# Performance work log

Measured on AMD Instinct MI355X. Metric: run time of the kernel, lower is better.

The kernel has to match this reference:

```python
import jax, jax.numpy as jnp
import numpy as np

# norse default LIFParameters (dt=1e-3): tau_mem_inv=100, tau_syn_inv=200, v_leak=0, v_reset=0
DT = 1e-3
TAU_MEM_INV = 100.0
TAU_SYN_INV = 200.0
V_TH_ENC = 1.0   # encoder built with default LIFParameters -> v_th=1.0
V_TH = 0.33      # LIF cells built with v_th=0.33
SEQ_LEN = 24
ALPHA = 100.0    # SuperSpike surrogate-gradient slope (norse 'super' method)

@jax.custom_vjp
def heaviside(x):
    # forward: hard threshold; backward: SuperSpike surrogate 1/(alpha*|x|+1)^2
    return (x > 0).astype(x.dtype)

def _hv_fwd(x):
    return heaviside(x), x

def _hv_bwd(x, g):
    return (g / (ALPHA * jnp.abs(x) + 1.0) ** 2,)

heaviside.defvjp(_hv_fwd, _hv_bwd)


def setup_inputs() -> dict:
    key = jax.random.key(0)
    ks = jax.random.split(key, 6)
    B, F, H, C = 4096, 1024, 256, 10
    def lin(k, fan_out, fan_in):  # torch Linear default init (no bias)
        bound = 1.0 / np.sqrt(fan_in)
        return jax.random.uniform(k, (fan_out, fan_in), jnp.float32, -bound, bound)
    return {
        "x": jax.random.normal(ks[0], (B, F), jnp.float32),
        "W1": lin(ks[1], H, F),
        "W2": lin(ks[2], H, H),
        "W3": lin(ks[3], H, H),
        "Wout": jax.random.normal(ks[4], (C, H), jnp.float32) * np.sqrt(2.0 / H),
        "feature_scalar": jnp.ones((1,), jnp.float32),
        "encoder_scalar": jnp.ones((1,), jnp.float32),
    }


def _lif_step(z_in, v, i):
    # norse lif_feed_forward_step: decay v/i from old state, spike, reset, then inject input into i
    v_dec = v + DT * TAU_MEM_INV * (-v + i)
    i_dec = i * (1.0 - DT * TAU_SYN_INV)
    z = heaviside(v_dec - V_TH)
    v_new = (1.0 - z) * v_dec  # v_reset = 0
    i_new = i_dec + z_in
    return z, v_new, i_new


def reference(x, W1, W2, W3, Wout, feature_scalar, encoder_scalar):
    B, F = x.shape
    H = W1.shape[0]
    C = Wout.shape[0]
    current = 2.0 * feature_scalar * x  # constant injected current, [B, F]
    z0 = lambda d: jnp.zeros((B, d), x.dtype)
    init = (z0(F), z0(H), z0(H), z0(H), z0(H), z0(H), z0(H), z0(C), z0(C))

    def step(state, _):
        v_enc, v1, i1, v2, i2, v3, i3, v_li, i_li = state
        # ConstantCurrentLIFEncoder (lif_current_encoder, v_th=1.0)
        v_enc = v_enc + DT * TAU_MEM_INV * (-v_enc + current)
        s = heaviside(v_enc - V_TH_ENC)
        v_enc = v_enc - s * v_enc  # reset to 0
        z = 5.0 * encoder_scalar * s
        # three Linear(no bias)+LIF stages (dropout in eval mode = identity)
        z, v1, i1 = _lif_step(1.2 * (z @ W1.T), v1, i1)
        z, v2, i2 = _lif_step(1.2 * (z @ W2.T), v2, i2)
        z, v3, i3 = _lif_step(1.2 * (z @ W3.T), v3, i3)
        # LILinearCell: leaky integrator readout
        v_li = v_li + DT * TAU_MEM_INV * (-v_li + i_li)
        i_li = i_li * (1.0 - DT * TAU_SYN_INV) + z @ Wout.T
        return (v_enc, v1, i1, v2, i2, v3, i3, v_li, i_li), None

    final, _ = jax.lax.scan(step, init, None, length=SEQ_LEN)
    return final[7]  # decode = voltages[-1], shape [B, n_classes]
```

## Files before the change

kernel.cpp:

```cpp
#include <hip/hip_runtime.h>

using u16 = unsigned short;
using u32 = unsigned int;
using u64 = unsigned long long;

typedef _Float16 half8 __attribute__((ext_vector_type(8)));
typedef float  f32x4 __attribute__((ext_vector_type(4)));
typedef u32    u32x4 __attribute__((ext_vector_type(4)));
typedef u32    u32x2 __attribute__((ext_vector_type(2)));

#define T_STEPS 24
#define NB 4096
#define NF 1024
#define NH 256
#define NCLS 10

static __device__ __forceinline__ void f16split(float w, u16& hi, u16& lo) {
  _Float16 h = (_Float16)w;
  float hf = (float)h;
  if (__builtin_fabsf(hf) < 6.103515625e-05f) { h = (_Float16)0.0f; hf = 0.0f; }
  float r = __fmul_rn(__fsub_rn(w, hf), 4096.0f);
  _Float16 l = (_Float16)r;
  hi = __builtin_bit_cast(u16, h);
  lo = __builtin_bit_cast(u16, l);
}

__global__ __launch_bounds__(256) void k_prep(const float* __restrict__ W1,
                                              const float* __restrict__ W2,
                                              const float* __restrict__ W3,
                                              u16* __restrict__ W1hl,
                                              u16* __restrict__ W2hl,
                                              u16* __restrict__ W3hl) {
  int blk = blockIdx.x, tid = threadIdx.x;
  const float* src; u16* dst; int K; int g;
  if (blk < 1024)      { src = W1; dst = W1hl; K = 1024; g = blk * 256 + tid; }
  else if (blk < 1280) { src = W2; dst = W2hl; K = 256;  g = (blk - 1024) * 256 + tid; }
  else                 { src = W3; dst = W3hl; K = 256;  g = (blk - 1280) * 256 + tid; }
  int n = g / K, k = g - n * K;
  u16 hi, lo;
  f16split(src[g], hi, lo);
  int p = k >> 6, j = k & 63;
  u16* d = dst + (size_t)n * 2 * K + p * 128 + j;
  d[0] = hi;
  d[64] = lo;
}

template <int NSC, int ASTRIDE>
__device__ __forceinline__ void mega_phase(u16* __restrict__ Bs,
                                           const u32* __restrict__ alds,
                                           const u16* __restrict__ wsrc,
                                           u32* __restrict__ zdst,
                                           float scale,
                                           int wid, int lane, int wm, int wn) {
  constexpr int KTOT = NSC * 32;
  constexpr int NG   = NSC / 4;

  const int q   = lane >> 4;
  const int bsh = q * 8;

  const u16* gs = wsrc + (size_t)(wid * 32 + (lane >> 2)) * KTOT + (lane & 3) * 8;
  const int sdst = wid * 1024;

  auto stage = [&](int s) {
    const int slot = s & 3;
    const u16* g = gs + s * 32;
    #pragma unroll
    for (int r = 0; r < 2; ++r)
      __builtin_amdgcn_global_load_lds(
          (const __attribute__((address_space(1))) u32*)(g + (size_t)r * 16 * KTOT),
          (__attribute__((address_space(3))) u32*)&Bs[slot * 8192 + sdst + r * 512],
          16, 0, 0);
  };

  auto waitv = [&](int n) {
    if (n == 4)      asm volatile("s_waitcnt vmcnt(4)" ::: "memory");
    else if (n == 2) asm volatile("s_waitcnt vmcnt(2)" ::: "memory");
    else             asm volatile("s_waitcnt vmcnt(0)" ::: "memory");
  };

  const int bru = (wn * 64 + (lane & 15)) * 32 + q * 8;

  int arow[3];
  #pragma unroll
  for (int ms = 0; ms < 3; ++ms)
    arow[ms] = (wm * 48 + ms * 16 + (lane & 15)) * ASTRIDE;

  auto expand = [&](u32 word) -> half8 {
    u32 by = (word >> bsh) & 0xFFu;
    u32 sp = by * 0x8001u;
    u32x4 d;
    d.x = (sp & 0x10001u) * 0x3C00u;
    d.y = ((sp >> 2) & 0x10001u) * 0x3C00u;
    d.z = ((sp >> 4) & 0x10001u) * 0x3C00u;
    d.w = ((sp >> 6) & 0x10001u) * 0x3C00u;
    return __builtin_bit_cast(half8, d);
  };

  const _Float16 scl = (_Float16)2.44140625e-4f;
  const half8 sc8 = {scl, scl, scl, scl, scl, scl, scl, scl};

  f32x4 acc[3][4];
  #pragma unroll
  for (int ms = 0; ms < 3; ++ms)
    #pragma unroll
    for (int ns = 0; ns < 4; ++ns)
      #pragma unroll
      for (int i = 0; i < 4; ++i) acc[ms][ns][i] = 0.0f;

  half8 afr[3][2];

  auto body = [&](int s, int j, int wcnt, bool dostage) {
    waitv(wcnt);
    __builtin_amdgcn_s_barrier();
    asm volatile("" ::: "memory");
    if (dostage) stage(s + 3);
    if (j == 0) {
      #pragma unroll
      for (int ms = 0; ms < 3; ++ms) {
        u32x2 bw = *(const u32x2*)(alds + arow[ms] + (s >> 2) * 2);
        afr[ms][0] = expand(bw.x);
        afr[ms][1] = expand(bw.y);
      }
    } else if (j == 2) {
      #pragma unroll
      for (int ms = 0; ms < 3; ++ms) {
        afr[ms][0] = afr[ms][0] * sc8;
        afr[ms][1] = afr[ms][1] * sc8;
      }
    }
    const int sel  = j & 1;
    const int slot = s & 3;
    half8 bfr[4];
    #pragma unroll
    for (int ns = 0; ns < 4; ++ns)
      bfr[ns] = *(const half8*)&Bs[slot * 8192 + bru + ns * 512];
    __builtin_amdgcn_s_setprio(1);
    #pragma unroll
    for (int ns = 0; ns < 4; ++ns)
      #pragma unroll
      for (int ms = 0; ms < 3; ++ms)
        acc[ms][ns] = __builtin_amdgcn_mfma_f32_16x16x32_f16(afr[ms][sel], bfr[ns],
                                                             acc[ms][ns], 0, 0, 0);
    __builtin_amdgcn_s_setprio(0);
  };

  stage(0); stage(1); stage(2);

  #pragma unroll 2
  for (int g = 0; g < NG - 1; ++g) {
    body(4 * g + 0, 0, 4, true);
    body(4 * g + 1, 1, 4, true);
    body(4 * g + 2, 2, 4, true);
    body(4 * g + 3, 3, 4, true);
  }
  {
    const int g = NG - 1;
    body(4 * g + 0, 0, 4, true);
    body(4 * g + 1, 1, 4, false);
    body(4 * g + 2, 2, 2, false);
    body(4 * g + 3, 3, 0, false);
  }
  __syncthreads();

  float* reg = (float*)Bs + wid * 1600;
  const int c16 = lane & 15;
  const int b2  = lane >> 5, c = lane & 31;

  #pragma unroll
  for (int r = 0; r < 2; ++r) {
    #pragma unroll
    for (int ms = 0; ms < 3; ++ms)
      #pragma unroll
      for (int j = 0; j < 2; ++j)
        #pragma unroll
        for (int i = 0; i < 4; ++i)
          reg[(ms * 16 + q * 4 + i) * 33 + j * 16 + c16] =
              __fmul_rn(scale, acc[ms][2 * r + j][i]);
    float v = 0.0f, ii = 0.0f;
    u32 zw = 0;
    #pragma unroll
    for (int t = 0; t < T_STEPS; ++t) {
      float cv = reg[(b2 * 24 + t) * 33 + c];
      float vdec = __fadd_rn(v, __fmul_rn(0.1f, __fsub_rn(ii, v)));
      float idec = __fmul_rn(0.8f, ii);
      bool z = vdec > 0.33f;
      v = z ? 0.0f : vdec;
      ii = __fadd_rn(idec, cv);
      zw |= ((u32)z) << t;
    }
    #pragma unroll
    for (int t = 0; t < T_STEPS; ++t) {
      u64 m = __ballot((zw >> t) & 1u);
      if (c == 0)
        zdst[((wm * 2 + b2) * 24 + t) * 8 + wn * 2 + r] = (u32)(m >> (b2 * 32));
    }
  }
  __syncthreads();
}

__global__ __launch_bounds__(512, 4) void k_mega(const float* __restrict__ x,
                                                 const float* __restrict__ fsp,
                                                 const float* __restrict__ esp,
                                                 const u16* __restrict__ W1hl,
                                                 const u16* __restrict__ W2hl,
                                                 const u16* __restrict__ W3hl,
                                                 const float* __restrict__ Wo,
                                                 float* __restrict__ out) {
  __shared__ __align__(16) u16 Bs[4 * 8192];
  __shared__ u32 zE[96 * 34];
  __shared__ u32 zA[96 * 8];

  const int tid  = threadIdx.x;
  const int wid  = tid >> 6;
  const int lane = tid & 63;
  const int wm   = wid & 1;
  const int wn   = wid >> 1;
  const int b0   = blockIdx.x * 4;

  {
    const int bb = wid >> 1;
    const int fbase = (wid & 1) * 512;
    const float c2 = __fmul_rn(2.0f, fsp[0]);
    float cur[8], v[8];
    #pragma unroll
    for (int j = 0; j < 8; ++j) {
      cur[j] = __fmul_rn(c2, x[(size_t)(b0 + bb) * 1024 + fbase + j * 64 + lane]);
      v[j] = 0.0f;
    }
    #pragma unroll
    for (int t = 0; t < T_STEPS; ++t) {
      #pragma unroll
      for (int j = 0; j < 8; ++j) {
        v[j] = __fadd_rn(v[j], __fmul_rn(0.1f, __fsub_rn(cur[j], v[j])));
        bool s = v[j] > 1.0f;
        if (s) v[j] = 0.0f;
        u64 m = __ballot(s);
        if (lane == 0) {
          int w0 = (bb * 24 + t) * 34 + (fbase >> 5) + 2 * j;
          zE[w0] = (u32)m;
          zE[w0 + 1] = (u32)(m >> 32);
        }
      }
    }
  }
  __syncthreads();

  const float s1 = __fmul_rn(1.2f, __fmul_rn(5.0f, esp[0]));
  mega_phase<64, 34>(Bs, zE, W1hl, zA, s1, wid, lane, wm, wn);
  mega_phase<16, 8>(Bs, zA, W2hl, zE, 1.2f, wid, lane, wm, wn);
  mega_phase<16, 8>(Bs, zE, W3hl, zA, 1.2f, wid, lane, wm, wn);

  {
    float* s_lds = (float*)Bs;
    #pragma unroll
    for (int r = 0; r < 2; ++r) {
      const int idx = tid + r * 512;
      const int b = idx >> 8, h = idx & 255;
      const u32* zp = zA + (b * 24) * 8 + (h >> 5);
      const int bit = h & 31;
      float p9 = 1.0f, p8 = 1.0f, s = 0.0f;
      #pragma unroll
      for (int e = 0; e < 24; ++e) {
        const float a = __fsub_rn(p9, p8);
        const u32 word = zp[(23 - e) * 8];
        s = __fadd_rn(s, ((word >> bit) & 1u) ? a : 0.0f);
        p9 = __fmul_rn(p9, 0.9f);
        p8 = __fmul_rn(p8, 0.8f);
      }
      s_lds[idx] = s;
    }
    __syncthreads();
    #pragma unroll
    for (int oi = 0; oi < 5; ++oi) {
      const int o = wid * 5 + oi;
      const int b = o / 10, cls = o - (o / 10) * 10;
      f32x4 sv = *(const f32x4*)&s_lds[b * 256 + lane * 4];
      f32x4 wv = *(const f32x4*)&Wo[(size_t)cls * 256 + lane * 4];
      float d = __fadd_rn(__fadd_rn(__fmul_rn(sv.x, wv.x), __fmul_rn(sv.y, wv.y)),
                          __fadd_rn(__fmul_rn(sv.z, wv.z), __fmul_rn(sv.w, wv.w)));
      #pragma unroll
      for (int off2 = 32; off2 >= 1; off2 >>= 1)
        d = __fadd_rn(d, __shfl_down(d, off2));
      if (lane == 0) out[(size_t)(b0 + b) * NCLS + cls] = d;
    }
  }
}

extern "C" void kernel_launch(void* const* d_in, const int* in_sizes, int n_in,
                              void* d_out, int out_size, void* d_ws, size_t ws_size,
                              hipStream_t stream) {
  const float* x  = (const float*)d_in[0];
  const float* W1 = (const float*)d_in[1];
  const float* W2 = (const float*)d_in[2];
  const float* W3 = (const float*)d_in[3];
  const float* Wo = (const float*)d_in[4];
  const float* fs = (const float*)d_in[5];
  const float* es = (const float*)d_in[6];

  char* ws = (char*)d_ws;
  const size_t off_w1 = 0;
  const size_t off_w2 = off_w1 + (size_t)NH * 2 * NF * 2;
  const size_t off_w3 = off_w2 + (size_t)NH * 2 * NH * 2;
  const size_t need   = off_w3 + (size_t)NH * 2 * NH * 2;
  if (ws_size < need) return;

  u16* W1hl = (u16*)(ws + off_w1);
  u16* W2hl = (u16*)(ws + off_w2);
  u16* W3hl = (u16*)(ws + off_w3);

  k_prep<<<dim3(1536), dim3(256), 0, stream>>>(W1, W2, W3, W1hl, W2hl, W3hl);
  k_mega<<<dim3(NB / 4), dim3(512), 0, stream>>>(x, fs, es, W1hl, W2hl, W3hl, Wo,
                                                 (float*)d_out);
}
```

Baseline: 246.2 us.

## Switch weight staging to swizzled double-buffered LDS and narrow LIF epilogue

Replaces the 4-slot, 3-stage-ahead weight prefetch ring with a 2-slot double buffer that syncs every k-step. This halves the B staging shared memory, which may allow more resident blocks per CU. It applies an XOR swizzle to the staged weight layout so the MFMA operand reads avoid LDS bank conflicts. The LIF epilogue now works on 16-column slices with a smaller padded scratch and writes 16-bit spike masks. The trade-off is a shallower prefetch and a full barrier per step, which could expose global load latency.

```diff
diff --git a/kernel.cpp b/kernel.cpp
--- a/kernel.cpp
+++ b/kernel.cpp
@@ -57,33 +57,29 @@
 
   const int q   = lane >> 4;
   const int bsh = q * 8;
-
-  const u16* gs = wsrc + (size_t)(wid * 32 + (lane >> 2)) * KTOT + (lane & 3) * 8;
-  const int sdst = wid * 1024;
+  const int c16 = lane & 15;
+
+  const u16* gs = wsrc + (size_t)(wid * 32 + (lane >> 2)) * KTOT
+                       + (((lane & 3) ^ ((lane >> 3) & 3)) * 8);
+  const int ldsw = wid * 1024;
 
   auto stage = [&](int s) {
-    const int slot = s & 3;
     const u16* g = gs + s * 32;
+    const int so = (s & 1) * 8192 + ldsw;
     #pragma unroll
     for (int r = 0; r < 2; ++r)
       __builtin_amdgcn_global_load_lds(
           (const __attribute__((address_space(1))) u32*)(g + (size_t)r * 16 * KTOT),
-          (__attribute__((address_space(3))) u32*)&Bs[slot * 8192 + sdst + r * 512],
+          (__attribute__((address_space(3))) u32*)&Bs[so + r * 512],
           16, 0, 0);
   };
 
-  auto waitv = [&](int n) {
-    if (n == 4)      asm volatile("s_waitcnt vmcnt(4)" ::: "memory");
-    else if (n == 2) asm volatile("s_waitcnt vmcnt(2)" ::: "memory");
-    else             asm volatile("s_waitcnt vmcnt(0)" ::: "memory");
-  };
-
-  const int bru = (wn * 64 + (lane & 15)) * 32 + q * 8;
+  const int bru = (wn * 64 + c16) * 32 + ((q ^ ((c16 >> 1) & 3)) * 8);
 
   int arow[3];
   #pragma unroll
   for (int ms = 0; ms < 3; ++ms)
-    arow[ms] = (wm * 48 + ms * 16 + (lane & 15)) * ASTRIDE;
+    arow[ms] = (wm * 48 + ms * 16 + c16) * ASTRIDE;
 
   auto expand = [&](u32 word) -> half8 {
     u32 by = (word >> bsh) & 0xFFu;
@@ -107,80 +103,63 @@
       #pragma unroll
       for (int i = 0; i < 4; ++i) acc[ms][ns][i] = 0.0f;
 
+  stage(0);
+
   half8 afr[3][2];
-
-  auto body = [&](int s, int j, int wcnt, bool dostage) {
-    waitv(wcnt);
-    __builtin_amdgcn_s_barrier();
-    asm volatile("" ::: "memory");
-    if (dostage) stage(s + 3);
-    if (j == 0) {
-      #pragma unroll
-      for (int ms = 0; ms < 3; ++ms) {
-        u32x2 bw = *(const u32x2*)(alds + arow[ms] + (s >> 2) * 2);
-        afr[ms][0] = expand(bw.x);
-        afr[ms][1] = expand(bw.y);
-      }
-    } else if (j == 2) {
-      #pragma unroll
-      for (int ms = 0; ms < 3; ++ms) {
-        afr[ms][0] = afr[ms][0] * sc8;
-        afr[ms][1] = afr[ms][1] * sc8;
-      }
-    }
-    const int sel  = j & 1;
-    const int slot = s & 3;
-    half8 bfr[4];
-    #pragma unroll
-    for (int ns = 0; ns < 4; ++ns)
-      bfr[ns] = *(const half8*)&Bs[slot * 8192 + bru + ns * 512];
-    __builtin_amdgcn_s_setprio(1);
-    #pragma unroll
-    for (int ns = 0; ns < 4; ++ns)
-      #pragma unroll
-      for (int ms = 0; ms < 3; ++ms)
-        acc[ms][ns] = __builtin_amdgcn_mfma_f32_16x16x32_f16(afr[ms][sel], bfr[ns],
-                                                             acc[ms][ns], 0, 0, 0);
-    __builtin_amdgcn_s_setprio(0);
-  };
-
-  stage(0); stage(1); stage(2);
-
   #pragma unroll 2
-  for (int g = 0; g < NG - 1; ++g) {
-    body(4 * g + 0, 0, 4, true);
-    body(4 * g + 1, 1, 4, true);
-    body(4 * g + 2, 2, 4, true);
-    body(4 * g + 3, 3, 4, true);
-  }
-  {
-    const int g = NG - 1;
-    body(4 * g + 0, 0, 4, true);
-    body(4 * g + 1, 1, 4, false);
-    body(4 * g + 2, 2, 2, false);
-    body(4 * g + 3, 3, 0, false);
+  for (int p = 0; p < NG; ++p) {
+    #pragma unroll
+    for (int j = 0; j < 4; ++j) {
+      const int s = 4 * p + j;
+      __syncthreads();
+      if (s + 1 < NSC) stage(s + 1);
+      if (j == 0) {
+        #pragma unroll
+        for (int ms = 0; ms < 3; ++ms) {
+          u32x2 bw = *(const u32x2*)(alds + arow[ms] + 2 * p);
+          afr[ms][0] = expand(bw.x);
+          afr[ms][1] = expand(bw.y);
+        }
+      } else if (j == 2) {
+        #pragma unroll
+        for (int ms = 0; ms < 3; ++ms) {
+          afr[ms][0] = afr[ms][0] * sc8;
+          afr[ms][1] = afr[ms][1] * sc8;
+        }
+      }
+      const int sel = j & 1;
+      const int so  = (s & 1) * 8192;
+      half8 bfr[4];
+      #pragma unroll
+      for (int ns = 0; ns < 4; ++ns)
+        bfr[ns] = *(const half8*)&Bs[so + bru + ns * 512];
+      __builtin_amdgcn_s_setprio(1);
+      #pragma unroll
+      for (int ns = 0; ns < 4; ++ns)
+        #pragma unroll
+        for (int ms = 0; ms < 3; ++ms)
+          acc[ms][ns] = __builtin_amdgcn_mfma_f32_16x16x32_f16(afr[ms][sel], bfr[ns],
+                                                               acc[ms][ns], 0, 0, 0);
+      __builtin_amdgcn_s_setprio(0);
+    }
   }
   __syncthreads();
 
-  float* reg = (float*)Bs + wid * 1600;
-  const int c16 = lane & 15;
-  const int b2  = lane >> 5, c = lane & 31;
+  float* reg = (float*)Bs + wid * 816;
+  const int b2 = (lane >> 4) & 1;
 
   #pragma unroll
-  for (int r = 0; r < 2; ++r) {
+  for (int r = 0; r < 4; ++r) {
     #pragma unroll
     for (int ms = 0; ms < 3; ++ms)
       #pragma unroll
-      for (int j = 0; j < 2; ++j)
-        #pragma unroll
-        for (int i = 0; i < 4; ++i)
-          reg[(ms * 16 + q * 4 + i) * 33 + j * 16 + c16] =
-              __fmul_rn(scale, acc[ms][2 * r + j][i]);
+      for (int i = 0; i < 4; ++i)
+        reg[(ms * 16 + q * 4 + i) * 17 + c16] = __fmul_rn(scale, acc[ms][r][i]);
     float v = 0.0f, ii = 0.0f;
     u32 zw = 0;
     #pragma unroll
     for (int t = 0; t < T_STEPS; ++t) {
-      float cv = reg[(b2 * 24 + t) * 33 + c];
+      float cv = reg[(b2 * 24 + t) * 17 + c16];
       float vdec = __fadd_rn(v, __fmul_rn(0.1f, __fsub_rn(ii, v)));
       float idec = __fmul_rn(0.8f, ii);
       bool z = vdec > 0.33f;
@@ -191,8 +170,10 @@
     #pragma unroll
     for (int t = 0; t < T_STEPS; ++t) {
       u64 m = __ballot((zw >> t) & 1u);
-      if (c == 0)
-        zdst[((wm * 2 + b2) * 24 + t) * 8 + wn * 2 + r] = (u32)(m >> (b2 * 32));
+      if (lane == b2 * 16) {
+        u16 val = (u16)(m >> (b2 * 16));
+        ((u16*)&zdst[((wm * 2 + b2) * 24 + t) * 8 + wn * 2 + (r >> 1)])[r & 1] = val;
+      }
     }
   }
   __syncthreads();
@@ -206,7 +187,7 @@
                                                  const u16* __restrict__ W3hl,
                                                  const float* __restrict__ Wo,
                                                  float* __restrict__ out) {
-  __shared__ __align__(16) u16 Bs[4 * 8192];
+  __shared__ __align__(16) u16 Bs[2 * 8192];
   __shared__ u32 zE[96 * 34];
   __shared__ u32 zA[96 * 8];
 
```

New measurement: 277.5 us. 12.7% more time.
